# Kernel tuning notes

Measured on AMD Instinct MI355X. Metric: run time of the kernel, lower is better.

## Reference

```python
import math
import jax, jax.numpy as jnp
import numpy as np

N_ANGLES = 180  # len(thetas), thetas = k*pi/180 for k in 0..179
IMG_SIZE = 256
BATCH = 2


def setup_inputs() -> dict:
    key = jax.random.key(0)
    image = jax.random.normal(key, (BATCH, 1, IMG_SIZE, IMG_SIZE), dtype=jnp.float32)
    return {"image": image}


def _bilinear_gather(flat_img, yi, xi, S, dtype):
    # flat_img: (B, S*S); yi, xi: (A, S, S) int32 corner indices
    valid = (xi >= 0) & (xi < S) & (yi >= 0) & (yi < S)
    idx = jnp.clip(yi, 0, S - 1) * S + jnp.clip(xi, 0, S - 1)
    v = jnp.take(flat_img, idx.reshape(-1), axis=1).reshape((flat_img.shape[0],) + idx.shape)
    return v * valid.astype(dtype)  # zeros padding_mode


def reference(image):
    # Radon.forward with circle=False: pad image to diagonal size, rotate
    # sampling grid per angle, grid_sample (bilinear, align_corners=True,
    # padding_mode='zeros'), sum over rows -> sinogram (B, 1, S, n_angles).
    B, _, S0, _ = image.shape
    S = int(math.ceil(math.sqrt(2.0) * S0))  # padded size (363 for 256)
    pad_total = S - S0
    pb, pa = pad_total // 2, pad_total - pad_total // 2
    img = jnp.pad(image[:, 0], ((0, 0), (pb, pa), (pb, pa)))  # (B, S, S)

    thetas = jnp.arange(N_ANGLES, dtype=jnp.float32) * jnp.float32(np.pi / N_ANGLES)
    cos = jnp.cos(thetas)[:, None, None]  # (A,1,1)
    sin = jnp.sin(thetas)[:, None, None]

    # affine_grid(align_corners=True) base grid in [-1, 1]
    lin = jnp.linspace(-1.0, 1.0, S, dtype=jnp.float32)
    x = lin[None, None, :]  # width coord
    y = lin[None, :, None]  # height coord
    gx = cos * x + sin * y   # (A, S, S) sample x
    gy = -sin * x + cos * y  # (A, S, S) sample y

    # grid_sample align_corners=True pixel coordinates
    ix = (gx + 1.0) * 0.5 * (S - 1)
    iy = (gy + 1.0) * 0.5 * (S - 1)
    x0 = jnp.floor(ix)
    y0 = jnp.floor(iy)
    wx = ix - x0
    wy = iy - y0
    x0i = x0.astype(jnp.int32)
    y0i = y0.astype(jnp.int32)

    flat = img.reshape(B, S * S)
    dt = img.dtype
    v00 = _bilinear_gather(flat, y0i, x0i, S, dt)
    v01 = _bilinear_gather(flat, y0i, x0i + 1, S, dt)
    v10 = _bilinear_gather(flat, y0i + 1, x0i, S, dt)
    v11 = _bilinear_gather(flat, y0i + 1, x0i + 1, S, dt)

    samp = (v00 * (1 - wx) * (1 - wy) + v01 * wx * (1 - wy)
            + v10 * (1 - wx) * wy + v11 * wx * wy)  # (B, A, S, S)

    sino = samp.sum(axis=2)             # sum over rows -> (B, A, S)
    return sino.transpose(0, 2, 1)[:, None]  # (B, 1, S, A)
```

## Files before the change

kernel.cpp:

```cpp
#include <hip/hip_runtime.h>

#define N_ANGLES 180
#define IMG 256
#define SPAD 363
#define PB 53
#define BATCH 2
#define TOTAL (BATCH * N_ANGLES * SPAD)
#define RSPLIT 4
#define NBLK ((TOTAL + 63) / 64)
#define NPAD 2048

#define QB 6
#define QDIM (IMG + 2 * QB)
#define QELEMS (QDIM * QDIM)
#define NTAB (2 * BATCH)
#define COFF ((QB - PB) * (QDIM + 1))

__global__ __launch_bounds__(256) void prep_quad(const float* __restrict__ img,
                                                 float4* __restrict__ quad) {
    const int e = blockIdx.x * 256 + threadIdx.x;
    if (e >= NTAB * QELEMS) return;
    const int xq = e % QDIM;
    const int t2 = e / QDIM;
    const int yq = t2 % QDIM;
    const int tb = t2 / QDIM;
    const int b  = tb & (BATCH - 1);
    const int v  = tb >> 1;
    const int x = xq - QB, y = yq - QB;
    const float* ib = img + b * (IMG * IMG);
    auto val = [&](int yy, int xx) -> float {
        if ((unsigned)yy >= (unsigned)IMG || (unsigned)xx >= (unsigned)IMG) return 0.0f;
        return v ? ib[xx * IMG + yy]
                 : ib[yy * IMG + xx];
    };
    float4 q;
    q.x = val(y, x);     q.y = val(y, x + 1);
    q.z = val(y + 1, x); q.w = val(y + 1, x + 1);
    quad[e] = q;
}

#define SAMP(r, A)                                                             \
    {                                                                          \
        const float rf = (float)(r);                                           \
        const float ix = fmaf(rf, stepA, v0A);                                 \
        const float iy = fmaf(rf, stepB, v0B);                                 \
        const float wx = ix - floorf(ix);         \
        const float wy = iy - floorf(iy);                                      \
        const int   xi = (int)ix;                \
        const int   yi = (int)iy;                                              \
        const float4 q = qt[yi * QDIM + xi + COFF];                            \
        const float omwx = 1.0f - wx;                                          \
        const float omwy = 1.0f - wy;                                          \
        const float top = fmaf(q.y, wx, q.x * omwx);                           \
        const float bot = fmaf(q.w, wx, q.z * omwx);                           \
        A = fmaf(bot, wy, fmaf(top, omwy, A));                                 \
    }

__global__ __launch_bounds__(256) void radon_quad(const float4* __restrict__ quad,
                                                  float* __restrict__ out) {
    const int L  = blockIdx.x;
    const int ob = (L & 7) * (NPAD / 8) + (L >> 3);
    if (ob >= NBLK) return;
    const int o = ob * 64 + (threadIdx.x >> 2);
    const int p = threadIdx.x & 3;
    if (o >= TOTAL) return;

    const int t = o % SPAD;
    const int g = o / SPAD;
    const int j = g % 180;
    const int b = g / 180;
    const int a = j + (j < 46 ? 0 : (j < 91 ? 89 : -45));
    const bool useT = (j >= 91);

    const float theta = (float)a * 0.017453292519943295f;
    float s, c;
    sincosf(theta, &s, &c);

    const float d  = 2.0f / 362.0f;
    const float lt = fmaf((float)t, d, -1.0f);
    const float ct  = c * lt;
    const float mst = -s * lt;

    const float sA = useT ? c   : s;
    const float cA = useT ? mst : ct;
    const float sB = useT ? s   : c;
    const float cB = useT ? ct  : mst;
    const float4* __restrict__ qt = quad + ((useT ? BATCH : 0) + b) * QELEMS;

    const float fA = sA * 181.0f, gA = (cA + 1.0f) * 181.0f;
    const float fB = sB * 181.0f, gB = (cB + 1.0f) * 181.0f;
    const float v0A = fmaf(fA, -1.0f, gA), stepA = fA * d;
    const float v0B = fmaf(fB, -1.0f, gB), stepB = fB * d;

    float rlo = 0.0f, rhi = 362.0f;
    {
        const float lo = 51.0f, hi = 310.0f;
        if (fabsf(stepA) < 1e-5f) {
            if (v0A < lo || v0A > hi) { rlo = 363.0f; rhi = -1.0f; }
        } else {
            const float r0 = (lo - v0A) / stepA;
            const float r1 = (hi - v0A) / stepA;
            rlo = fmaxf(rlo, fminf(r0, r1));
            rhi = fminf(rhi, fmaxf(r0, r1));
        }
        if (fabsf(stepB) < 1e-5f) {
            if (v0B < lo || v0B > hi) { rlo = 363.0f; rhi = -1.0f; }
        } else {
            const float r0 = (lo - v0B) / stepB;
            const float r1 = (hi - v0B) / stepB;
            rlo = fmaxf(rlo, fminf(r0, r1));
            rhi = fminf(rhi, fmaxf(r0, r1));
        }
    }
    const int rmin = max(0,   (int)floorf(rlo));
    const int rmax = min(362, (int)ceilf(rhi));

    float acc0 = 0.0f, acc1 = 0.0f;
    int r = rmin + ((p - rmin) & 3);
#pragma unroll 2
    for (; r + 4 <= rmax; r += 8) {
        SAMP(r, acc0);
        SAMP(r + 4, acc1);
    }
    if (r <= rmax) SAMP(r, acc0);
    float acc = acc0 + acc1;

    acc += __shfl_xor(acc, 1);
    acc += __shfl_xor(acc, 2);

    if (p == 0) {
        out[(b * SPAD + t) * N_ANGLES + a] = acc;
    }
}


__global__ __launch_bounds__(256) void transpose_kernel(const float* __restrict__ img,
                                                        float* __restrict__ imgT) {
    __shared__ float tile[32][33];
    const int b  = blockIdx.z;
    const int tx = blockIdx.x * 32;
    const int ty = blockIdx.y * 32;
    const int lx = threadIdx.x & 31;
    const int l8 = threadIdx.x >> 5;
    const float* ib = img  + b * IMG * IMG;
    float*       ob = imgT + b * IMG * IMG;
#pragma unroll
    for (int i = 0; i < 4; ++i) {
        const int ly = l8 + i * 8;
        tile[ly][lx] = ib[(ty + ly) * IMG + tx + lx];
    }
    __syncthreads();
#pragma unroll
    for (int i = 0; i < 4; ++i) {
        const int ly = l8 + i * 8;
        ob[(tx + ly) * IMG + ty + lx] = tile[lx][ly];
    }
}

#define SAMPLE(r, CHECKED)                                                     \
    {                                                                          \
        const float lr  = fmaf((float)(r), d, -1.0f);                          \
        const float ix  = fmaf(fA, lr, gA);                                    \
        const float iy  = fmaf(fB, lr, gB);                                    \
        const float wx  = ix - floorf(ix);                                     \
        const float wy  = iy - floorf(iy);                                     \
        const int   xi  = (int)ix;                                             \
        const int   yi  = (int)iy;                                             \
        float v00, v01, v10, v11;                                              \
        if (CHECKED) {                                                         \
            const int xA = xi - PB, yA = yi - PB;                              \
            const bool vx0 = (unsigned)xA       < (unsigned)IMG;               \
            const bool vx1 = (unsigned)(xA + 1) < (unsigned)IMG;               \
            const bool vy0 = (unsigned)yA       < (unsigned)IMG;               \
            const bool vy1 = (unsigned)(yA + 1) < (unsigned)IMG;               \
            const float* rp = base + yA * IMG + xA;                            \
            v00 = (vx0 && vy0) ? rp[0]       : 0.0f;                           \
            v01 = (vx1 && vy0) ? rp[1]       : 0.0f;                           \
            v10 = (vx0 && vy1) ? rp[IMG]     : 0.0f;                           \
            v11 = (vx1 && vy1) ? rp[IMG + 1] : 0.0f;                           \
        } else {                                                               \
            const float* rp = base + (yi * IMG + xi - (PB * IMG + PB));        \
            v00 = rp[0]; v01 = rp[1]; v10 = rp[IMG]; v11 = rp[IMG + 1];        \
        }                                                                      \
        const float omwx = 1.0f - wx;                                          \
        const float omwy = 1.0f - wy;                                          \
        const float top  = fmaf(v01, wx, v00 * omwx);                          \
        const float bot  = fmaf(v11, wx, v10 * omwx);                          \
        acc = fmaf(bot, wy, fmaf(top, omwy, acc));                             \
    }

template <bool HAVE_T>
__global__ __launch_bounds__(256) void radon_kernel(const float* __restrict__ img,
                                                    const float* __restrict__ imgT,
                                                    float* __restrict__ out) {
    const int gid = blockIdx.x * 256 + threadIdx.x;
    const int o = gid >> 1;
    const int p = gid & 1;
    if (o >= TOTAL) return;

    const int t  = o % SPAD;
    const int ba = o / SPAD;
    const int a  = ba % N_ANGLES;
    const int b  = ba / N_ANGLES;

    const float theta = (float)a * 0.017453292519943295f;
    float s, c;
    sincosf(theta, &s, &c);

    const float d  = 2.0f / 362.0f;
    const float lt = fmaf((float)t, d, -1.0f);
    const float ct  = c * lt;
    const float mst = -s * lt;

    const bool useT = HAVE_T && (s > fabsf(c));
    const float sA = useT ? c   : s;
    const float cA = useT ? mst : ct;
    const float sB = useT ? s   : c;
    const float cB = useT ? ct  : mst;
    const float* __restrict__ base = (useT ? imgT : img) + b * (IMG * IMG);

    const float fA = sA * 181.0f;
    const float gA = (cA + 1.0f) * 181.0f;
    const float fB = sB * 181.0f;
    const float gB = (cB + 1.0f) * 181.0f;

    const float v0A = fmaf(fA, -1.0f, gA), dvA = fA * d;
    const float v0B = fmaf(fB, -1.0f, gB), dvB = fB * d;

    auto clip = [](float v0, float dv, float lo, float hi, float& rlo, float& rhi) {
        if (fabsf(dv) < 1e-5f) {
            if (v0 < lo || v0 > hi) { rlo = 363.0f; rhi = -1.0f; }
        } else {
            const float r0 = (lo - v0) / dv;
            const float r1 = (hi - v0) / dv;
            rlo = fmaxf(rlo, fminf(r0, r1));
            rhi = fminf(rhi, fmaxf(r0, r1));
        }
    };

    float rloA = 0.0f, rhiA = 362.0f;
    clip(v0A, dvA, 51.0f, 310.0f, rloA, rhiA);
    clip(v0B, dvB, 51.0f, 310.0f, rloA, rhiA);
    const int rmin = max(0,   (int)floorf(rloA));
    const int rmax = min(362, (int)ceilf(rhiA));

    float rloI = (float)rmin, rhiI = (float)rmax;
    clip(v0A, dvA, 54.0f, 307.0f, rloI, rhiI);
    clip(v0B, dvB, 54.0f, 307.0f, rloI, rhiI);
    int rin_lo = (int)ceilf(rloI);
    int rin_hi = (int)floorf(rhiI);
    if (rin_lo < rmin) rin_lo = rmin;
    if (rin_hi > rmax) rin_hi = rmax;
    if (rin_lo > rin_hi) { rin_lo = rmax + 1; rin_hi = rmax; }

    float acc = 0.0f;
    for (int r = rmin + ((p - rmin) & 1); r < rin_lo; r += 2)
        SAMPLE(r, true);
#pragma unroll 2
    for (int r = rin_lo + ((p - rin_lo) & 1); r <= rin_hi; r += 2)
        SAMPLE(r, false);
    for (int r = rin_hi + 1 + ((p - rin_hi - 1) & 1); r <= rmax; r += 2)
        SAMPLE(r, true);

    acc += __shfl_xor(acc, 1);

    if (p == 0) {
        out[(b * SPAD + t) * N_ANGLES + a] = acc;
    }
}

extern "C" void kernel_launch(void* const* d_in, const int* in_sizes, int n_in,
                              void* d_out, int out_size, void* d_ws, size_t ws_size,
                              hipStream_t stream) {
    const float* img = (const float*)d_in[0];
    float* out = (float*)d_out;

    const size_t needQ = (size_t)NTAB * QELEMS * sizeof(float4);
    if (ws_size >= needQ) {
        float4* quad = (float4*)d_ws;
        prep_quad<<<(NTAB * QELEMS + 255) / 256, 256, 0, stream>>>(img, quad);
        radon_quad<<<NPAD, 256, 0, stream>>>(quad, out);
    } else if (ws_size >= (size_t)(BATCH * IMG * IMG * sizeof(float))) {
        float* imgT = (float*)d_ws;
        transpose_kernel<<<dim3(8, 8, 2), 256, 0, stream>>>(img, imgT);
        const int threads = TOTAL * 2;
        radon_kernel<true><<<(threads + 255) / 256, 256, 0, stream>>>(img, imgT, out);
    } else {
        const int threads = TOTAL * 2;
        radon_kernel<false><<<(threads + 255) / 256, 256, 0, stream>>>(img, nullptr, out);
    }
}
```

Baseline: 95.27 us.

## Interleave batch quads and share sample geometry across both batch images

The precomputed bilinear quad table now interleaves the two batch images per texel. Each thread computes the sampling coordinates and weights once and accumulates both batch outputs from two adjacent float4 loads. The ray split goes from 4 to 8 lanes per output so the halved thread count still fills the device. This removes duplicated coordinate math and index work across batches, at the cost of more register pressure and a longer shuffle reduction.

```diff
diff --git a/kernel.cpp b/kernel.cpp
--- a/kernel.cpp
+++ b/kernel.cpp
@@ -6,69 +6,71 @@
 #define PB 53
 #define BATCH 2
 #define TOTAL (BATCH * N_ANGLES * SPAD)
-#define RSPLIT 4
-#define NBLK ((TOTAL + 63) / 64)
+#define GEOM (N_ANGLES * SPAD)
+#define RSPLIT 8
+#define NBLK2 ((GEOM + 31) / 32)
 #define NPAD 2048
 
 #define QB 6
 #define QDIM (IMG + 2 * QB)
 #define QELEMS (QDIM * QDIM)
-#define NTAB (2 * BATCH)
 #define COFF ((QB - PB) * (QDIM + 1))
 
-__global__ __launch_bounds__(256) void prep_quad(const float* __restrict__ img,
-                                                 float4* __restrict__ quad) {
-    const int e = blockIdx.x * 256 + threadIdx.x;
-    if (e >= NTAB * QELEMS) return;
-    const int xq = e % QDIM;
-    const int t2 = e / QDIM;
-    const int yq = t2 % QDIM;
-    const int tb = t2 / QDIM;
-    const int b  = tb & (BATCH - 1);
-    const int v  = tb >> 1;
+__global__ __launch_bounds__(256) void prep_quad2(const float* __restrict__ img,
+                                                  float4* __restrict__ quad) {
+    const int n = blockIdx.x * 256 + threadIdx.x;
+    if (n >= 2 * QELEMS) return;
+    const int xq = n % QDIM;
+    const int yq = (n / QDIM) % QDIM;
+    const int v  = n / QELEMS;
     const int x = xq - QB, y = yq - QB;
-    const float* ib = img + b * (IMG * IMG);
-    auto val = [&](int yy, int xx) -> float {
-        if ((unsigned)yy >= (unsigned)IMG || (unsigned)xx >= (unsigned)IMG) return 0.0f;
-        return v ? ib[xx * IMG + yy]
-                 : ib[yy * IMG + xx];
-    };
-    float4 q;
-    q.x = val(y, x);     q.y = val(y, x + 1);
-    q.z = val(y + 1, x); q.w = val(y + 1, x + 1);
-    quad[e] = q;
-}
-
-#define SAMP(r, A)                                                             \
+#pragma unroll
+    for (int b = 0; b < BATCH; ++b) {
+        const float* ib = img + b * (IMG * IMG);
+        auto val = [&](int yy, int xx) -> float {
+            if ((unsigned)yy >= (unsigned)IMG || (unsigned)xx >= (unsigned)IMG) return 0.0f;
+            return v ? ib[xx * IMG + yy] : ib[yy * IMG + xx];
+        };
+        float4 q;
+        q.x = val(y, x);     q.y = val(y, x + 1);
+        q.z = val(y + 1, x); q.w = val(y + 1, x + 1);
+        quad[n * 2 + b] = q;
+    }
+}
+
+#define SAMP2(r, A0, A1)                                                       \
     {                                                                          \
         const float rf = (float)(r);                                           \
         const float ix = fmaf(rf, stepA, v0A);                                 \
         const float iy = fmaf(rf, stepB, v0B);                                 \
         const float wx = ix - floorf(ix);         \
         const float wy = iy - floorf(iy);                                      \
-        const int   xi = (int)ix;                \
+        const int   xi = (int)ix;                                              \
         const int   yi = (int)iy;                                              \
-        const float4 q = qt[yi * QDIM + xi + COFF];                            \
+        const float4* e = qt + 2 * (yi * QDIM + xi) + 2 * COFF;                \
+        const float4 q0 = e[0];                                                \
+        const float4 q1 = e[1];                                                \
         const float omwx = 1.0f - wx;                                          \
         const float omwy = 1.0f - wy;                                          \
-        const float top = fmaf(q.y, wx, q.x * omwx);                           \
-        const float bot = fmaf(q.w, wx, q.z * omwx);                           \
-        A = fmaf(bot, wy, fmaf(top, omwy, A));                                 \
-    }
-
-__global__ __launch_bounds__(256) void radon_quad(const float4* __restrict__ quad,
-                                                  float* __restrict__ out) {
+        const float t0 = fmaf(q0.y, wx, q0.x * omwx);                          \
+        const float b0 = fmaf(q0.w, wx, q0.z * omwx);                          \
+        A0 = fmaf(b0, wy, fmaf(t0, omwy, A0));                                 \
+        const float t1 = fmaf(q1.y, wx, q1.x * omwx);                          \
+        const float b1 = fmaf(q1.w, wx, q1.z * omwx);                          \
+        A1 = fmaf(b1, wy, fmaf(t1, omwy, A1));                                 \
+    }
+
+__global__ __launch_bounds__(256) void radon_quad2(const float4* __restrict__ quad,
+                                                   float* __restrict__ out) {
     const int L  = blockIdx.x;
     const int ob = (L & 7) * (NPAD / 8) + (L >> 3);
-    if (ob >= NBLK) return;
-    const int o = ob * 64 + (threadIdx.x >> 2);
-    const int p = threadIdx.x & 3;
-    if (o >= TOTAL) return;
-
-    const int t = o % SPAD;
-    const int g = o / SPAD;
-    const int j = g % 180;
-    const int b = g / 180;
+    if (ob >= NBLK2) return;
+    const int o2 = ob * 32 + (threadIdx.x >> 3);
+    const int p  = threadIdx.x & 7;
+    if (o2 >= GEOM) return;
+
+    const int t = o2 % SPAD;
+    const int j = o2 / SPAD;
     const int a = j + (j < 46 ? 0 : (j < 91 ? 89 : -45));
     const bool useT = (j >= 91);
 
@@ -85,7 +87,7 @@
     const float cA = useT ? mst : ct;
     const float sB = useT ? s   : c;
     const float cB = useT ? ct  : mst;
-    const float4* __restrict__ qt = quad + ((useT ? BATCH : 0) + b) * QELEMS;
+    const float4* __restrict__ qt = quad + (useT ? 2 * QELEMS : 0);
 
     const float fA = sA * 181.0f, gA = (cA + 1.0f) * 181.0f;
     const float fB = sB * 181.0f, gB = (cB + 1.0f) * 181.0f;
@@ -115,21 +117,28 @@
     const int rmin = max(0,   (int)floorf(rlo));
     const int rmax = min(362, (int)ceilf(rhi));
 
-    float acc0 = 0.0f, acc1 = 0.0f;
-    int r = rmin + ((p - rmin) & 3);
-#pragma unroll 2
-    for (; r + 4 <= rmax; r += 8) {
-        SAMP(r, acc0);
-        SAMP(r + 4, acc1);
-    }
-    if (r <= rmax) SAMP(r, acc0);
-    float acc = acc0 + acc1;
-
-    acc += __shfl_xor(acc, 1);
-    acc += __shfl_xor(acc, 2);
+    float a00 = 0.0f, a01 = 0.0f;
+    float a10 = 0.0f, a11 = 0.0f;
+    int r = rmin + ((p - rmin) & 7);
+    for (; r + 8 <= rmax; r += 16) {
+        SAMP2(r,     a00, a10);
+        SAMP2(r + 8, a01, a11);
+    }
+    if (r <= rmax) SAMP2(r, a00, a10);
+    float accB0 = a00 + a01;
+    float accB1 = a10 + a11;
+
+    accB0 += __shfl_xor(accB0, 1);
+    accB0 += __shfl_xor(accB0, 2);
+    accB0 += __shfl_xor(accB0, 4);
+    accB1 += __shfl_xor(accB1, 1);
+    accB1 += __shfl_xor(accB1, 2);
+    accB1 += __shfl_xor(accB1, 4);
 
     if (p == 0) {
-        out[(b * SPAD + t) * N_ANGLES + a] = acc;
+        const int base = t * N_ANGLES + a;
+        out[base] = accB0;
+        out[base + SPAD * N_ANGLES] = accB1;
     }
 }
 
@@ -275,11 +284,11 @@
     const float* img = (const float*)d_in[0];
     float* out = (float*)d_out;
 
-    const size_t needQ = (size_t)NTAB * QELEMS * sizeof(float4);
+    const size_t needQ = (size_t)(2 * QELEMS) * 2 * sizeof(float4);
     if (ws_size >= needQ) {
         float4* quad = (float4*)d_ws;
-        prep_quad<<<(NTAB * QELEMS + 255) / 256, 256, 0, stream>>>(img, quad);
-        radon_quad<<<NPAD, 256, 0, stream>>>(quad, out);
+        prep_quad2<<<(2 * QELEMS + 255) / 256, 256, 0, stream>>>(img, quad);
+        radon_quad2<<<NPAD, 256, 0, stream>>>(quad, out);
     } else if (ws_size >= (size_t)(BATCH * IMG * IMG * sizeof(float))) {
         float* imgT = (float*)d_ws;
         transpose_kernel<<<dim3(8, 8, 2), 256, 0, stream>>>(img, imgT);
```

Measured after the change: 99.56 us. +4.5%, slower.
